# Performance work log

Hardware: AMD Instinct MI355X
Metric: run time of the kernel (lower is better)

Reference implementation:

```python
import jax, jax.numpy as jnp
import numpy as np

EPS = 1e-6

def _normalize(A):
    # zero the diagonal, add self-loops
    n = A.shape[-1]
    eye = jnp.eye(n, dtype=A.dtype)
    A_hat = A * (1.0 - eye) + eye  # [B,N,N]
    # symmetric degree normalization with eps inside as in the TF code:
    # d = 1/(eps + sqrt(rowsum)); norm = diag(d) @ A_hat @ diag(d)
    d = 1.0 / (EPS + jnp.sqrt(jnp.sum(A_hat, axis=2)))  # [B,N]
    return A_hat * d[:, :, None] * d[:, None, :]


def setup_inputs() -> dict:
    key = jax.random.key(0)
    k1, k2, k3 = jax.random.split(key, 3)
    B, N, F, O = 8, 2048, 128, 128
    x = jax.random.normal(k1, (B, N, F), dtype=jnp.float32)
    adj = jax.random.uniform(k2, (B, N, N), dtype=jnp.float32)
    kernel = jax.random.normal(k3, (F, O), dtype=jnp.float32) * 0.05
    return {"x": x, "adj": adj, "kernel": kernel}


def reference(x, adj, kernel):
    norm = _normalize(adj)                      # [B,N,N]
    agg = jnp.einsum('bnm,bmf->bnf', norm, x)   # batch_dot
    out = jnp.einsum('bnf,fo->bno', agg, kernel)
    return jax.nn.relu(out)
```

## Files before the change

### kernel.cpp

```cpp
#include <hip/hip_runtime.h>


typedef __bf16 bf16x8 __attribute__((ext_vector_type(8)));
typedef float  f32x4  __attribute__((ext_vector_type(4)));

#define NN 2048
#define NB 8

__device__ __forceinline__ void load_lds16(__bf16* lds, const __bf16* g) {
    __builtin_amdgcn_global_load_lds(
        (const __attribute__((address_space(1))) void*)g,
        (__attribute__((address_space(3))) void*)lds, 16, 0, 0);
}

__global__ __launch_bounds__(256) void wt_kernel(const float* __restrict__ W,
                                                 __bf16* __restrict__ Wt) {
    int idx = blockIdx.x * 256 + threadIdx.x;
    int f = idx >> 7, o = idx & 127;
    Wt[o * 128 + f] = (__bf16)W[idx];
}

__global__ __launch_bounds__(256) void d_kernel(const float* __restrict__ adj,
                                                float* __restrict__ dvec) {
    const int lane = threadIdx.x & 63;
    const int row  = blockIdx.x * 4 + (threadIdx.x >> 6);
    const float* rp = adj + (size_t)row * NN;
    float4 s4 = {0.f, 0.f, 0.f, 0.f};
#pragma unroll
    for (int it = 0; it < 8; ++it) {
        float4 v = *(const float4*)(rp + it * 256 + lane * 4);
        s4.x += v.x; s4.y += v.y; s4.z += v.z; s4.w += v.w;
    }
    float s = (s4.x + s4.y) + (s4.z + s4.w);
#pragma unroll
    for (int off = 32; off; off >>= 1) s += __shfl_down(s, off);
    if (lane == 0) {
        int n = row & (NN - 1);
        float sh = s - rp[n] + 1.0f;
        dvec[row] = 1.0f / (1e-6f + sqrtf(sh));
    }
}

template <int KTOT, bool IS_XW>
__global__ __launch_bounds__(256) void gemm_kernel(
    const float* __restrict__ A, const __bf16* __restrict__ Bmat,
    const float* __restrict__ dvec, float* __restrict__ out,
    __bf16* __restrict__ yt) {
    __shared__ alignas(16) __bf16 sA[64][40];
    __shared__ alignas(16) __bf16 sB[128][32];

    const int tid  = threadIdx.x;
    const int wave = tid >> 6;
    const int lane = tid & 63;
    const int b    = blockIdx.y;
    const int n_local_base = blockIdx.x * 64;
    const int row_base = b * NN + n_local_base;

    const __bf16* Bptr = IS_XW ? Bmat : (Bmat + (size_t)b * 128 * KTOT);

    const int a_row = tid >> 2;
    const int a_col = (tid & 3) * 8;
    const float* a_src = A + (size_t)(row_base + a_row) * KTOT + a_col;

    f32x4 acc[8];
#pragma unroll
    for (int i = 0; i < 8; ++i) acc[i] = (f32x4){0.f, 0.f, 0.f, 0.f};

    f32x4 a0 = *(const f32x4*)(a_src);
    f32x4 a1 = *(const f32x4*)(a_src + 4);

    const int NITER = KTOT / 32;
    for (int kt = 0; kt < NITER; ++kt) {
        float av[8] = {a0.x, a0.y, a0.z, a0.w, a1.x, a1.y, a1.z, a1.w};
        if constexpr (!IS_XW) {
            int n  = n_local_base + a_row;
            int m0 = kt * 32 + a_col;
#pragma unroll
            for (int j = 0; j < 8; ++j)
                if (m0 + j == n) av[j] = 1.0f;
        }
        bf16x8 apack;
#pragma unroll
        for (int j = 0; j < 8; ++j) apack[j] = (__bf16)av[j];
        *(bf16x8*)(&sA[a_row][a_col]) = apack;

        {
            int row0 = wave * 32;
            const __bf16* src0 =
                Bptr + (size_t)(row0 + (lane >> 2)) * KTOT + kt * 32 + (lane & 3) * 8;
            load_lds16(&sB[row0][0], src0);
            load_lds16(&sB[row0 + 16][0], src0 + (size_t)16 * KTOT);
        }
        __syncthreads();

        if (kt + 1 < NITER) {
            a0 = *(const f32x4*)(a_src + (size_t)(kt + 1) * 32);
            a1 = *(const f32x4*)(a_src + (size_t)(kt + 1) * 32 + 4);
        }

        bf16x8 af = *(const bf16x8*)(&sA[wave * 16 + (lane & 15)][(lane >> 4) * 8]);
#pragma unroll
        for (int nb = 0; nb < 8; ++nb) {
            bf16x8 bf = *(const bf16x8*)(&sB[nb * 16 + (lane & 15)][(lane >> 4) * 8]);
            acc[nb] = __builtin_amdgcn_mfma_f32_16x16x32_bf16(af, bf, acc[nb], 0, 0, 0);
        }
        __syncthreads();
    }

    const int col0 = lane & 15;
    const int rq   = (lane >> 4) * 4;
#pragma unroll
    for (int r = 0; r < 4; ++r) {
        int grow = row_base + wave * 16 + rq + r;
        float dr = dvec[grow];
        if constexpr (IS_XW) {
            int m_loc = grow - b * NN;
#pragma unroll
            for (int nb = 0; nb < 8; ++nb) {
                int o = nb * 16 + col0;
                yt[((size_t)b * 128 + o) * NN + m_loc] = (__bf16)(acc[nb][r] * dr);
            }
        } else {
#pragma unroll
            for (int nb = 0; nb < 8; ++nb) {
                int o = nb * 16 + col0;
                float v = acc[nb][r] * dr;
                out[(size_t)grow * 128 + o] = v > 0.f ? v : 0.f;
            }
        }
    }
}

extern "C" void kernel_launch(void* const* d_in, const int* in_sizes, int n_in,
                              void* d_out, int out_size, void* d_ws, size_t ws_size,
                              hipStream_t stream) {
    const float* x   = (const float*)d_in[0];
    const float* adj = (const float*)d_in[1];
    const float* W   = (const float*)d_in[2];
    float* out = (float*)d_out;

    char* ws = (char*)d_ws;
    float*  dvec = (float*)ws;
    __bf16* yt   = (__bf16*)(ws + 65536);
    __bf16* Wt   = (__bf16*)(ws + 65536 + (size_t)NB * 128 * NN * 2);

    hipLaunchKernelGGL(wt_kernel, dim3(64), dim3(256), 0, stream, W, Wt);
    hipLaunchKernelGGL(d_kernel, dim3(NB * NN / 4), dim3(256), 0, stream, adj, dvec);
    hipLaunchKernelGGL((gemm_kernel<128, true>), dim3(32, NB), dim3(256), 0, stream,
                       x, Wt, dvec, (float*)nullptr, yt);
    hipLaunchKernelGGL((gemm_kernel<2048, false>), dim3(32, NB), dim3(256), 0, stream,
                       adj, yt, dvec, out, (__bf16*)nullptr);
}
```

Before: 246.3 us.

## Double-buffer LDS tiles and halve GEMM row tile to 32 for more blocks

The GEMM kernel now uses 32-row tiles instead of 64 and launches 512 one-dimensional blocks, with the batch index interleaved into blockIdx. The four waves split the output 2x2, each computing 16 rows by 64 columns. LDS buffers for A and B are double-buffered: the next B tile is prefetched asynchronously into the other buffer, which removes the trailing barrier from each iteration. This aims to raise occupancy and overlap memory with MFMA on the bandwidth-bound adj pass. The cost is that the B operand is loaded twice as often relative to output work.

```diff
diff --git a/kernel.cpp b/kernel.cpp
--- a/kernel.cpp
+++ b/kernel.cpp
@@ -2,6 +2,7 @@
 
 
 typedef __bf16 bf16x8 __attribute__((ext_vector_type(8)));
+typedef __bf16 bf16x4 __attribute__((ext_vector_type(4)));
 typedef float  f32x4  __attribute__((ext_vector_type(4)));
 
 #define NN 2048
@@ -46,84 +47,89 @@
     const float* __restrict__ A, const __bf16* __restrict__ Bmat,
     const float* __restrict__ dvec, float* __restrict__ out,
     __bf16* __restrict__ yt) {
-    __shared__ alignas(16) __bf16 sA[64][40];
-    __shared__ alignas(16) __bf16 sB[128][32];
+    __shared__ alignas(16) __bf16 sA[2][32][40];
+    __shared__ alignas(16) __bf16 sB[2][128][32];
 
     const int tid  = threadIdx.x;
     const int wave = tid >> 6;
     const int lane = tid & 63;
-    const int b    = blockIdx.y;
-    const int n_local_base = blockIdx.x * 64;
+    const int b    = blockIdx.x & 7;
+    const int tile = blockIdx.x >> 3;
+    const int n_local_base = tile * 32;
     const int row_base = b * NN + n_local_base;
 
     const __bf16* Bptr = IS_XW ? Bmat : (Bmat + (size_t)b * 128 * KTOT);
 
-    const int a_row = tid >> 2;
-    const int a_col = (tid & 3) * 8;
+    const int a_row = tid >> 3;
+    const int a_col = (tid & 7) * 4;
     const float* a_src = A + (size_t)(row_base + a_row) * KTOT + a_col;
 
-    f32x4 acc[8];
+    const int b_row0 = wave * 32;
+    const __bf16* b_src =
+        Bptr + (size_t)(b_row0 + (lane >> 2)) * KTOT + (lane & 3) * 8;
+
+    const int rsel = (wave & 1) * 16;
+    const int csel = (wave >> 1) * 64;
+
+    f32x4 acc[4];
 #pragma unroll
-    for (int i = 0; i < 8; ++i) acc[i] = (f32x4){0.f, 0.f, 0.f, 0.f};
+    for (int i = 0; i < 4; ++i) acc[i] = (f32x4){0.f, 0.f, 0.f, 0.f};
 
-    f32x4 a0 = *(const f32x4*)(a_src);
-    f32x4 a1 = *(const f32x4*)(a_src + 4);
+    f32x4 a = *(const f32x4*)(a_src);
+    load_lds16(&sB[0][b_row0][0], b_src);
+    load_lds16(&sB[0][b_row0 + 16][0], b_src + (size_t)16 * KTOT);
 
     const int NITER = KTOT / 32;
     for (int kt = 0; kt < NITER; ++kt) {
-        float av[8] = {a0.x, a0.y, a0.z, a0.w, a1.x, a1.y, a1.z, a1.w};
+        const int cur = kt & 1;
+        float av[4] = {a.x, a.y, a.z, a.w};
         if constexpr (!IS_XW) {
             int n  = n_local_base + a_row;
             int m0 = kt * 32 + a_col;
 #pragma unroll
-            for (int j = 0; j < 8; ++j)
+            for (int j = 0; j < 4; ++j)
                 if (m0 + j == n) av[j] = 1.0f;
         }
-        bf16x8 apack;
+        bf16x4 apack;
 #pragma unroll
-        for (int j = 0; j < 8; ++j) apack[j] = (__bf16)av[j];
-        *(bf16x8*)(&sA[a_row][a_col]) = apack;
+        for (int j = 0; j < 4; ++j) apack[j] = (__bf16)av[j];
+        *(bf16x4*)(&sA[cur][a_row][a_col]) = apack;
 
-        {
-            int row0 = wave * 32;
-            const __bf16* src0 =
-                Bptr + (size_t)(row0 + (lane >> 2)) * KTOT + kt * 32 + (lane & 3) * 8;
-            load_lds16(&sB[row0][0], src0);
-            load_lds16(&sB[row0 + 16][0], src0 + (size_t)16 * KTOT);
-        }
         __syncthreads();
 
         if (kt + 1 < NITER) {
-            a0 = *(const f32x4*)(a_src + (size_t)(kt + 1) * 32);
-            a1 = *(const f32x4*)(a_src + (size_t)(kt + 1) * 32 + 4);
+            const __bf16* bs = b_src + (size_t)(kt + 1) * 32;
+            load_lds16(&sB[cur ^ 1][b_row0][0], bs);
+            load_lds16(&sB[cur ^ 1][b_row0 + 16][0], bs + (size_t)16 * KTOT);
+            a = *(const f32x4*)(a_src + (size_t)(kt + 1) * 32);
         }
 
-        bf16x8 af = *(const bf16x8*)(&sA[wave * 16 + (lane & 15)][(lane >> 4) * 8]);
+        bf16x8 af = *(const bf16x8*)(&sA[cur][rsel + (lane & 15)][(lane >> 4) * 8]);
 #pragma unroll
-        for (int nb = 0; nb < 8; ++nb) {
-            bf16x8 bf = *(const bf16x8*)(&sB[nb * 16 + (lane & 15)][(lane >> 4) * 8]);
-            acc[nb] = __builtin_amdgcn_mfma_f32_16x16x32_bf16(af, bf, acc[nb], 0, 0, 0);
+        for (int nb = 0; nb < 4; ++nb) {
+            bf16x8 bfv = *(const bf16x8*)(
+                &sB[cur][csel + nb * 16 + (lane & 15)][(lane >> 4) * 8]);
+            acc[nb] = __builtin_amdgcn_mfma_f32_16x16x32_bf16(af, bfv, acc[nb], 0, 0, 0);
         }
-        __syncthreads();
     }
 
     const int col0 = lane & 15;
     const int rq   = (lane >> 4) * 4;
 #pragma unroll
     for (int r = 0; r < 4; ++r) {
-        int grow = row_base + wave * 16 + rq + r;
+        int grow = row_base + rsel + rq + r;
         float dr = dvec[grow];
         if constexpr (IS_XW) {
             int m_loc = grow - b * NN;
 #pragma unroll
-            for (int nb = 0; nb < 8; ++nb) {
-                int o = nb * 16 + col0;
+            for (int nb = 0; nb < 4; ++nb) {
+                int o = csel + nb * 16 + col0;
                 yt[((size_t)b * 128 + o) * NN + m_loc] = (__bf16)(acc[nb][r] * dr);
             }
         } else {
 #pragma unroll
-            for (int nb = 0; nb < 8; ++nb) {
-                int o = nb * 16 + col0;
+            for (int nb = 0; nb < 4; ++nb) {
+                int o = csel + nb * 16 + col0;
                 float v = acc[nb][r] * dr;
                 out[(size_t)grow * 128 + o] = v > 0.f ? v : 0.f;
             }
@@ -146,8 +152,8 @@
 
     hipLaunchKernelGGL(wt_kernel, dim3(64), dim3(256), 0, stream, W, Wt);
     hipLaunchKernelGGL(d_kernel, dim3(NB * NN / 4), dim3(256), 0, stream, adj, dvec);
-    hipLaunchKernelGGL((gemm_kernel<128, true>), dim3(32, NB), dim3(256), 0, stream,
+    hipLaunchKernelGGL((gemm_kernel<128, true>), dim3(512), dim3(256), 0, stream,
                        x, Wt, dvec, (float*)nullptr, yt);
-    hipLaunchKernelGGL((gemm_kernel<2048, false>), dim3(32, NB), dim3(256), 0, stream,
+    hipLaunchKernelGGL((gemm_kernel<2048, false>), dim3(512), dim3(256), 0, stream,
                        adj, yt, dvec, out, (__bf16*)nullptr);
 }
```

Result: no change. 249.2 us (+1.2%).
